# Kernel optimization log

Hardware: AMD Instinct MI355X
Metric: run time of the kernel (lower is better)

The kernel has to match this reference:

```python
import jax, jax.numpy as jnp
import numpy as np

K_PERIODS = 4   # k_periods
PMAX = 64       # pmax
MIN_P = 16      # min_period_threshold (already clamped to <= PMAX)


def setup_inputs() -> dict:
    key = jax.random.key(0)
    B, T, N = 32, 512, 128
    x = jax.random.normal(key, (B, T, N), dtype=jnp.float32)
    return {"x": x}


def reference(x):
    # x: [B, T, N]
    B, T, N = x.shape
    K = K_PERIODS
    seqs = jnp.transpose(x, (0, 2, 1)).reshape(B * N, T)  # [BN, T]

    # top-k nonzero frequencies by rFFT amplitude
    spec = jnp.fft.rfft(seqs, axis=-1)                    # [BN, T//2+1]
    amp = jnp.abs(spec)
    amp = amp.at[..., 0].set(0.0)                         # zero DC component
    kamp, kidx = jax.lax.top_k(amp, K)                    # [BN, K] each
    kidx = jnp.maximum(kidx, 1)

    # periods and cycle counts
    P = jnp.clip(T // kidx, MIN_P, PMAX)                  # [BN, K]
    cycles = jnp.maximum(T // P, 1)                       # [BN, K]
    take = cycles * P

    # static upper bound on cycles (torch uses data-dependent cycles.max();
    # extra trailing cycle slots here are fully masked to zero)
    Cmax = T // MIN_P
    idx_c = jnp.arange(Cmax)                              # [Cmax]
    idx_p = jnp.arange(PMAX)                              # [Pmax]

    base = jnp.maximum(T - take, 0)[..., None, None]      # [BN, K, 1, 1]
    indices = base + idx_c[None, None, :, None] * P[..., None, None] \
              + idx_p[None, None, None, :]                # [BN, K, Cmax, Pmax]
    indices = jnp.clip(indices, 0, T - 1)

    # gather: broadcast seqs over (K, Cmax)
    gathered = jnp.take_along_axis(seqs[:, None, None, :], indices, axis=-1)

    mask = ((idx_c[None, None, :, None] < cycles[..., None, None]) &
            (idx_p[None, None, None, :] < P[..., None, None])).astype(x.dtype)
    gathered = gathered * mask

    gathered = gathered.reshape(B, N, K, Cmax, PMAX)
    mask = mask.reshape(B, N, K, Cmax, PMAX)
    kamp = kamp.reshape(B, N, K)
    return gathered, mask, kamp
```

## Files before the change

### kernel.cpp

```cpp
#include <hip/hip_runtime.h>
#include <math.h>

#define TLEN 512
#define NCH  128
#define KP   4
#define PMAXV 64
#define CMAXV 32
#define MINP 16
#define NSEQ 4096
#define OUTG ((size_t)NSEQ * KP * CMAXV * PMAXV)

#define PAD8(i) ((i) + ((i) >> 3))
#define XP   580
#define SEQP 520

typedef float nfloat4 __attribute__((ext_vector_type(4)));

__global__ void twiddle_setup(double2* __restrict__ Wg) {
    const int j = threadIdx.x;
    double ang = -6.283185307179586476925286766559 * (double)j / (double)TLEN;
    double sv, cv;
    sincos(ang, &sv, &cv);
    Wg[j] = make_double2(cv, sv);
}

__global__ __launch_bounds__(256) void periodicity_kernel(
    const float* __restrict__ x,
    const double2* __restrict__ Wg,
    float* __restrict__ out_g,
    float* __restrict__ out_m,
    float* __restrict__ out_a)
{
    const int tid  = threadIdx.x;
    const int lane = tid & 63;
    const int w    = tid >> 6;
    const int s0   = blockIdx.x << 2;
    const int b    = s0 >> 7;
    const int n0   = s0 & (NCH - 1);

    __shared__ float   seqf[4 * SEQP];
    __shared__ double  re[4 * XP];
    __shared__ double  im[4 * XP];
    __shared__ double2 W[256];

    {
        const int col = tid & 3;
        const int t0  = tid >> 2;
        const float* base = x + (size_t)b * TLEN * NCH + n0 + col;
        #pragma unroll
        for (int it = 0; it < 8; ++it) {
            const int t = t0 + 64 * it;
            seqf[col * SEQP + t] = base[(size_t)t * NCH];
        }
        W[tid] = Wg[tid];
    }
    __syncthreads();

    float*  sf = seqf + w * SEQP;
    double* RE = re + w * XP;
    double* IM = im + w * XP;

    #pragma unroll
    for (int u = 0; u < 8; ++u) {
        const int i = lane + 64 * u;
        const int r = (int)(__brev((unsigned)i) >> 23);
        RE[PAD8(i)] = (double)sf[r];
        IM[PAD8(i)] = 0.0;
    }
    __builtin_amdgcn_wave_barrier();

    for (int st = 1; st <= 9; ++st) {
        const int half = 1 << (st - 1);
        #pragma unroll
        for (int u = 0; u < 4; ++u) {
            const int j   = lane + 64 * u;
            const int pos = j & (half - 1);
            const int i1  = ((j >> (st - 1)) << st) + pos;
            const int i2  = i1 + half;
            const double2 wv = W[pos << (9 - st)];
            const double ar = RE[PAD8(i1)], ai = IM[PAD8(i1)];
            const double cr = RE[PAD8(i2)], ci = IM[PAD8(i2)];
            const double tr = wv.x * cr - wv.y * ci;
            const double ti = wv.x * ci + wv.y * cr;
            RE[PAD8(i1)] = ar + tr;  IM[PAD8(i1)] = ai + ti;
            RE[PAD8(i2)] = ar - tr;  IM[PAD8(i2)] = ai - ti;
        }
        __builtin_amdgcn_wave_barrier();
    }

    #pragma unroll
    for (int u = 0; u < 4; ++u) {
        const int k = lane + 64 * u;
        const double xr = RE[PAD8(k)], xi = IM[PAD8(k)];
        RE[PAD8(k)] = (k == 0) ? 0.0 : (xr * xr + xi * xi);
    }
    if (lane == 0) {
        const double xr = RE[PAD8(256)], xi = IM[PAD8(256)];
        RE[PAD8(256)] = xr * xr + xi * xi;
    }
    __builtin_amdgcn_wave_barrier();

    double bv0, bv1, bv2, bv3;
    int    bi0, bi1, bi2, bi3;
    #pragma unroll
    for (int q = 0; q < KP; ++q) {
        double v  = RE[PAD8(lane)];
        int    vi = lane;
        #pragma unroll
        for (int u = 1; u < 4; ++u) {
            const double uu = RE[PAD8(lane + 64 * u)];
            if (uu > v) { v = uu; vi = lane + 64 * u; }
        }
        if (lane == 0) {
            const double uu = RE[PAD8(256)];
            if (uu > v) { v = uu; vi = 256; }
        }
        #pragma unroll
        for (int off = 32; off > 0; off >>= 1) {
            const double ov = __shfl_xor(v, off, 64);
            const int    oi = __shfl_xor(vi, off, 64);
            if (ov > v || (ov == v && oi < vi)) { v = ov; vi = oi; }
        }
        if (q == 0) { bv0 = v; bi0 = vi; }
        else if (q == 1) { bv1 = v; bi1 = vi; }
        else if (q == 2) { bv2 = v; bi2 = vi; }
        else { bv3 = v; bi3 = vi; }
        if (lane == 0) RE[PAD8(vi)] = -1.0;
        __builtin_amdgcn_wave_barrier();
    }

    int P0, P1, P2, P3, C0, C1, C2, C3, B0, B1, B2, B3;
    {
        int k0 = bi0 < 1 ? 1 : bi0;  P0 = TLEN / k0;
        P0 = P0 < MINP ? MINP : (P0 > PMAXV ? PMAXV : P0);
        C0 = TLEN / P0;  B0 = TLEN - C0 * P0;
        int k1 = bi1 < 1 ? 1 : bi1;  P1 = TLEN / k1;
        P1 = P1 < MINP ? MINP : (P1 > PMAXV ? PMAXV : P1);
        C1 = TLEN / P1;  B1 = TLEN - C1 * P1;
        int k2 = bi2 < 1 ? 1 : bi2;  P2 = TLEN / k2;
        P2 = P2 < MINP ? MINP : (P2 > PMAXV ? PMAXV : P2);
        C2 = TLEN / P2;  B2 = TLEN - C2 * P2;
        int k3 = bi3 < 1 ? 1 : bi3;  P3 = TLEN / k3;
        P3 = P3 < MINP ? MINP : (P3 > PMAXV ? PMAXV : P3);
        C3 = TLEN / P3;  B3 = TLEN - C3 * P3;
    }
    const int s = s0 + w;
    if (lane == 0) {
        out_a[(size_t)s * KP + 0] = (float)sqrt(bv0);
        out_a[(size_t)s * KP + 1] = (float)sqrt(bv1);
        out_a[(size_t)s * KP + 2] = (float)sqrt(bv2);
        out_a[(size_t)s * KP + 3] = (float)sqrt(bv3);
    }

    float* og = out_g + (size_t)s * (KP * CMAXV * PMAXV);
    float* om = out_m + (size_t)s * (KP * CMAXV * PMAXV);
    const int pp = (lane & 15) << 2;
    for (int r = lane >> 4; r < KP * CMAXV; r += 4) {
        const int k = r >> 5;
        const int c = r & (CMAXV - 1);
        const int P    = k == 0 ? P0 : k == 1 ? P1 : k == 2 ? P2 : P3;
        const int cyc  = k == 0 ? C0 : k == 1 ? C1 : k == 2 ? C2 : C3;
        const int base = k == 0 ? B0 : k == 1 ? B1 : k == 2 ? B2 : B3;
        nfloat4 g = (nfloat4)(0.f, 0.f, 0.f, 0.f);
        nfloat4 m = (nfloat4)(0.f, 0.f, 0.f, 0.f);
        if (c < cyc) {
            const int idx = base + c * P + pp;
            if (pp     < P) { g.x = sf[idx];     m.x = 1.f; }
            if (pp + 1 < P) { g.y = sf[idx + 1]; m.y = 1.f; }
            if (pp + 2 < P) { g.z = sf[idx + 2]; m.z = 1.f; }
            if (pp + 3 < P) { g.w = sf[idx + 3]; m.w = 1.f; }
        }
        *(nfloat4*)(og + r * PMAXV + pp) = g;
        *(nfloat4*)(om + r * PMAXV + pp) = m;
    }
}

extern "C" void kernel_launch(void* const* d_in, const int* in_sizes, int n_in,
                              void* d_out, int out_size, void* d_ws, size_t ws_size,
                              hipStream_t stream) {
    const float* x = (const float*)d_in[0];
    float* out = (float*)d_out;
    float* og = out;
    float* om = out + OUTG;
    float* oa = om + OUTG;
    double2* Wg = (double2*)d_ws;

    twiddle_setup<<<dim3(1), dim3(256), 0, stream>>>(Wg);
    periodicity_kernel<<<dim3(NSEQ / 4), dim3(256), 0, stream>>>(x, Wg, og, om, oa);
}
```

Before: 276.9 us.

## Fuse twiddle setup into main kernel, register top-k, split mask/gather stores

Each block now computes its FFT twiddle factors with sincos instead of reading them from a separate setup kernel, which removes one kernel launch and its dependency. The top-k search keeps the power spectrum in registers (5 values per lane) rather than re-reading LDS on each pass, removing the shared-memory writes and wave barriers. The output loop is split into a mask-only store pass followed by a gather store pass. The costs are redundant double-precision sincos in every block and a second loop over the output rows.

```diff
diff --git a/kernel.cpp b/kernel.cpp
--- a/kernel.cpp
+++ b/kernel.cpp
@@ -16,17 +16,8 @@
 
 typedef float nfloat4 __attribute__((ext_vector_type(4)));
 
-__global__ void twiddle_setup(double2* __restrict__ Wg) {
-    const int j = threadIdx.x;
-    double ang = -6.283185307179586476925286766559 * (double)j / (double)TLEN;
-    double sv, cv;
-    sincos(ang, &sv, &cv);
-    Wg[j] = make_double2(cv, sv);
-}
-
 __global__ __launch_bounds__(256) void periodicity_kernel(
     const float* __restrict__ x,
-    const double2* __restrict__ Wg,
     float* __restrict__ out_g,
     float* __restrict__ out_m,
     float* __restrict__ out_a)
@@ -52,7 +43,10 @@
             const int t = t0 + 64 * it;
             seqf[col * SEQP + t] = base[(size_t)t * NCH];
         }
-        W[tid] = Wg[tid];
+        double ang = -6.283185307179586476925286766559 * (double)tid / (double)TLEN;
+        double sv, cv;
+        sincos(ang, &sv, &cv);
+        W[tid] = make_double2(cv, sv);
     }
     __syncthreads();
 
@@ -88,33 +82,31 @@
         __builtin_amdgcn_wave_barrier();
     }
 
+    double a[5];
+    int    bins[5];
     #pragma unroll
     for (int u = 0; u < 4; ++u) {
         const int k = lane + 64 * u;
         const double xr = RE[PAD8(k)], xi = IM[PAD8(k)];
-        RE[PAD8(k)] = (k == 0) ? 0.0 : (xr * xr + xi * xi);
+        a[u]    = (k == 0) ? 0.0 : (xr * xr + xi * xi);
+        bins[u] = k;
     }
+    a[4]    = -1.0;
+    bins[4] = 256;
     if (lane == 0) {
         const double xr = RE[PAD8(256)], xi = IM[PAD8(256)];
-        RE[PAD8(256)] = xr * xr + xi * xi;
+        a[4] = xr * xr + xi * xi;
     }
-    __builtin_amdgcn_wave_barrier();
 
     double bv0, bv1, bv2, bv3;
     int    bi0, bi1, bi2, bi3;
     #pragma unroll
     for (int q = 0; q < KP; ++q) {
-        double v  = RE[PAD8(lane)];
-        int    vi = lane;
+        double v  = a[0];
+        int    vi = bins[0];
         #pragma unroll
-        for (int u = 1; u < 4; ++u) {
-            const double uu = RE[PAD8(lane + 64 * u)];
-            if (uu > v) { v = uu; vi = lane + 64 * u; }
-        }
-        if (lane == 0) {
-            const double uu = RE[PAD8(256)];
-            if (uu > v) { v = uu; vi = 256; }
-        }
+        for (int j = 1; j < 5; ++j)
+            if (a[j] > v) { v = a[j]; vi = bins[j]; }
         #pragma unroll
         for (int off = 32; off > 0; off >>= 1) {
             const double ov = __shfl_xor(v, off, 64);
@@ -125,8 +117,9 @@
         else if (q == 1) { bv1 = v; bi1 = vi; }
         else if (q == 2) { bv2 = v; bi2 = vi; }
         else { bv3 = v; bi3 = vi; }
-        if (lane == 0) RE[PAD8(vi)] = -1.0;
-        __builtin_amdgcn_wave_barrier();
+        #pragma unroll
+        for (int j = 0; j < 5; ++j)
+            if (bins[j] == vi) a[j] = -1.0;
     }
 
     int P0, P1, P2, P3, C0, C1, C2, C3, B0, B1, B2, B3;
@@ -155,6 +148,22 @@
     float* og = out_g + (size_t)s * (KP * CMAXV * PMAXV);
     float* om = out_m + (size_t)s * (KP * CMAXV * PMAXV);
     const int pp = (lane & 15) << 2;
+
+    for (int r = lane >> 4; r < KP * CMAXV; r += 4) {
+        const int k = r >> 5;
+        const int c = r & (CMAXV - 1);
+        const int P    = k == 0 ? P0 : k == 1 ? P1 : k == 2 ? P2 : P3;
+        const int cyc  = k == 0 ? C0 : k == 1 ? C1 : k == 2 ? C2 : C3;
+        nfloat4 m = (nfloat4)(0.f, 0.f, 0.f, 0.f);
+        if (c < cyc) {
+            m.x = (pp     < P) ? 1.f : 0.f;
+            m.y = (pp + 1 < P) ? 1.f : 0.f;
+            m.z = (pp + 2 < P) ? 1.f : 0.f;
+            m.w = (pp + 3 < P) ? 1.f : 0.f;
+        }
+        *(nfloat4*)(om + r * PMAXV + pp) = m;
+    }
+
     for (int r = lane >> 4; r < KP * CMAXV; r += 4) {
         const int k = r >> 5;
         const int c = r & (CMAXV - 1);
@@ -162,16 +171,14 @@
         const int cyc  = k == 0 ? C0 : k == 1 ? C1 : k == 2 ? C2 : C3;
         const int base = k == 0 ? B0 : k == 1 ? B1 : k == 2 ? B2 : B3;
         nfloat4 g = (nfloat4)(0.f, 0.f, 0.f, 0.f);
-        nfloat4 m = (nfloat4)(0.f, 0.f, 0.f, 0.f);
         if (c < cyc) {
             const int idx = base + c * P + pp;
-            if (pp     < P) { g.x = sf[idx];     m.x = 1.f; }
-            if (pp + 1 < P) { g.y = sf[idx + 1]; m.y = 1.f; }
-            if (pp + 2 < P) { g.z = sf[idx + 2]; m.z = 1.f; }
-            if (pp + 3 < P) { g.w = sf[idx + 3]; m.w = 1.f; }
+            if (pp     < P) g.x = sf[idx];
+            if (pp + 1 < P) g.y = sf[idx + 1];
+            if (pp + 2 < P) g.z = sf[idx + 2];
+            if (pp + 3 < P) g.w = sf[idx + 3];
         }
         *(nfloat4*)(og + r * PMAXV + pp) = g;
-        *(nfloat4*)(om + r * PMAXV + pp) = m;
     }
 }
 
@@ -183,8 +190,6 @@
     float* og = out;
     float* om = out + OUTG;
     float* oa = om + OUTG;
-    double2* Wg = (double2*)d_ws;
 
-    twiddle_setup<<<dim3(1), dim3(256), 0, stream>>>(Wg);
-    periodicity_kernel<<<dim3(NSEQ / 4), dim3(256), 0, stream>>>(x, Wg, og, om, oa);
+    periodicity_kernel<<<dim3(NSEQ / 4), dim3(256), 0, stream>>>(x, og, om, oa);
 }
```

Measured after the change: 273.2 us. No clear change (-1.3%).
